# Optimization experiments

Hardware: AMD Instinct MI355X
Metric: run time of the kernel (lower is better)

## Reference

```python
import jax, jax.numpy as jnp
import numpy as np

B = 64          # batch size
KP1 = 1024      # K + 1 (negatives + positive)
D_IN = 2048     # inputSize
D_PROJ = 512    # proj_dim
N_MEM = 81920   # outputSize * f_Num
T = 0.07        # temperature
MOMENTUM = 0.5


def _l2norm(x):
    # Normalize(2): x / ||x||_2 along last dim
    return x / jnp.sqrt(jnp.sum(x * x, axis=-1, keepdims=True))


def setup_inputs() -> dict:
    key = jax.random.key(0)
    k1, k2, k3, k4, k5 = jax.random.split(key, 5)
    stdv = 1.0 / np.sqrt(D_IN / 3)
    feat = jax.random.normal(k1, (B, D_IN), jnp.float32)
    y = jax.random.randint(k2, (B,), 0, N_MEM, dtype=jnp.int32)
    idx = jax.random.randint(k3, (B, KP1), 0, N_MEM, dtype=jnp.int32)
    memory = jax.random.uniform(k4, (N_MEM, D_IN), jnp.float32, -stdv, stdv)
    W = jax.random.normal(k5, (D_PROJ, D_IN), jnp.float32) / np.sqrt(D_IN)
    b = jnp.zeros((D_PROJ,), jnp.float32)
    return {"feat": feat, "y": y, "idx": idx, "memory": memory, "W": W, "b": b}


def reference(feat, y, idx, memory, W, b):
    # project + l2-normalize query features: [B, D_PROJ]
    feat_proj = _l2norm(feat @ W.T + b)
    # gather bank rows (detached in original): [B*KP1, D_IN]
    weight = memory[idx.reshape(-1)]
    weight_proj = _l2norm(weight @ W.T + b).reshape(B, KP1, D_PROJ)
    # bmm([B,KP1,D_PROJ], [B,D_PROJ,1]) / T -> [B, KP1, 1]
    out = (jnp.einsum('bkd,bd->bk', weight_proj, feat_proj) / T)[..., None]
    # momentum scatter-update of memory rows at y
    new_rows = MOMENTUM * memory[y] + (1.0 - MOMENTUM) * feat
    new_memory = memory.at[y].set(new_rows)
    return out, new_memory
```

## Files before the change

kernel.cpp:

```cpp
#include <hip/hip_runtime.h>


#define B_SZ     64
#define KP1      1024
#define D_IN     2048
#define D_PROJ   512
#define N_MEM    81920
#define INV_T    (1.0f / 0.07f)

typedef __bf16 bf16x8 __attribute__((ext_vector_type(8)));
typedef float  f32x4  __attribute__((ext_vector_type(4)));

__device__ __forceinline__ unsigned short f2bf(float f) {
    unsigned int u = __float_as_uint(f);
    unsigned int r = (u + 0x7FFFu + ((u >> 16) & 1u)) >> 16;
    return (unsigned short)r;
}

__global__ void cvt_w_kernel(const float* __restrict__ W, unsigned short* __restrict__ Wb) {
    int i = blockIdx.x * 256 + threadIdx.x;
    float4 v = ((const float4*)W)[i];
    ushort4 o;
    o.x = f2bf(v.x); o.y = f2bf(v.y); o.z = f2bf(v.z); o.w = f2bf(v.w);
    ((ushort4*)Wb)[i] = o;
}

__global__ void feat_proj_kernel(const float* __restrict__ feat,
                                 const float* __restrict__ W,
                                 const float* __restrict__ bias,
                                 float* __restrict__ fp_out) {
    const int b = blockIdx.x, tid = threadIdx.x;
    __shared__ float sF[D_IN];
    __shared__ float sP[D_PROJ];
    __shared__ float sRed[256];

    #pragma unroll
    for (int i = 0; i < D_IN / 256; ++i)
        sF[tid + i * 256] = feat[(long)b * D_IN + tid + i * 256];
    __syncthreads();

    float pv[2];
    #pragma unroll
    for (int pass = 0; pass < 2; ++pass) {
        const int n = tid + pass * 256;
        const float4* wr = (const float4*)(W + (long)n * D_IN);
        const float4* fr = (const float4*)sF;
        float s = 0.f;
        for (int j = 0; j < D_IN / 4; ++j) {
            float4 wv = wr[j], fv = fr[j];
            s += wv.x * fv.x + wv.y * fv.y + wv.z * fv.z + wv.w * fv.w;
        }
        pv[pass] = s + bias[n];
        sP[n] = pv[pass];
    }
    __syncthreads();
    sRed[tid] = pv[0] * pv[0] + pv[1] * pv[1];
    __syncthreads();
    for (int s = 128; s > 0; s >>= 1) {
        if (tid < s) sRed[tid] += sRed[tid + s];
        __syncthreads();
    }
    const float rn = rsqrtf(sRed[0]);
    fp_out[(long)b * D_PROJ + tid]       = pv[0] * rn;
    fp_out[(long)b * D_PROJ + tid + 256] = pv[1] * rn;
}

#define AS_STRIDE 72
__global__ __launch_bounds__(256, 2)
void main_gemm_kernel(const float* __restrict__ memory,
                      const int* __restrict__ idx,
                      const unsigned short* __restrict__ Wb,
                      const float* __restrict__ fp,
                      const float* __restrict__ bias,
                      float* __restrict__ out) {
    const int tid  = threadIdx.x;
    const int w    = tid >> 6;
    const int lane = tid & 63;
    const int quad = lane >> 4;
    const int c16  = lane & 15;
    const int blk  = blockIdx.x;
    const int b    = blk >> 4;

    __shared__ unsigned short As[64 * AS_STRIDE];
    __shared__ float sFP[D_PROJ];
    __shared__ float sBias[D_PROJ];
    __shared__ int   sIdx[64];
    __shared__ float sSS[4 * 64];
    __shared__ float sDot[4 * 64];

    for (int i = tid; i < D_PROJ; i += 256) {
        sFP[i]   = fp[(long)b * D_PROJ + i];
        sBias[i] = bias[i];
    }
    if (tid < 64) sIdx[tid] = idx[blk * 64 + tid];
    __syncthreads();

    f32x4 acc[4][8];
    const f32x4 zero = {0.f, 0.f, 0.f, 0.f};
    #pragma unroll
    for (int mt = 0; mt < 4; ++mt)
        #pragma unroll
        for (int nt = 0; nt < 8; ++nt) acc[mt][nt] = zero;

    const int  row  = tid >> 2;
    const int  q    = tid & 3;
    const long arow = (long)sIdx[row] * D_IN;

    for (int k0 = 0; k0 < D_IN; k0 += 64) {
        const float4* src = (const float4*)(memory + arow + k0 + q * 16);
        float4 v0 = src[0], v1 = src[1], v2 = src[2], v3 = src[3];

        __syncthreads();
        float f[16] = {v0.x, v0.y, v0.z, v0.w, v1.x, v1.y, v1.z, v1.w,
                       v2.x, v2.y, v2.z, v2.w, v3.x, v3.y, v3.z, v3.w};
        unsigned int pk[8];
        #pragma unroll
        for (int j = 0; j < 8; ++j)
            pk[j] = (unsigned int)f2bf(f[2 * j]) | ((unsigned int)f2bf(f[2 * j + 1]) << 16);
        uint4* dst = (uint4*)&As[row * AS_STRIDE + q * 16];
        dst[0] = make_uint4(pk[0], pk[1], pk[2], pk[3]);
        dst[1] = make_uint4(pk[4], pk[5], pk[6], pk[7]);
        __syncthreads();

        #pragma unroll
        for (int ks = 0; ks < 2; ++ks) {
            bf16x8 af[4];
            #pragma unroll
            for (int mt = 0; mt < 4; ++mt)
                af[mt] = *(const bf16x8*)&As[(mt * 16 + c16) * AS_STRIDE + ks * 32 + quad * 8];
            #pragma unroll
            for (int nt = 0; nt < 8; ++nt) {
                const int n = w * 128 + nt * 16 + c16;
                bf16x8 bfr = *(const bf16x8*)&Wb[(long)n * D_IN + k0 + ks * 32 + quad * 8];
                #pragma unroll
                for (int mt = 0; mt < 4; ++mt)
                    acc[mt][nt] = __builtin_amdgcn_mfma_f32_16x16x32_bf16(
                        af[mt], bfr, acc[mt][nt], 0, 0, 0);
            }
        }
    }

    float ssl[4][4], dtl[4][4];
    #pragma unroll
    for (int mt = 0; mt < 4; ++mt)
        #pragma unroll
        for (int r = 0; r < 4; ++r) { ssl[mt][r] = 0.f; dtl[mt][r] = 0.f; }

    #pragma unroll
    for (int nt = 0; nt < 8; ++nt) {
        const int n = w * 128 + nt * 16 + c16;
        const float bv = sBias[n], fv = sFP[n];
        #pragma unroll
        for (int mt = 0; mt < 4; ++mt)
            #pragma unroll
            for (int r = 0; r < 4; ++r) {
                const float P = acc[mt][nt][r] + bv;
                ssl[mt][r] += P * P;
                dtl[mt][r] += P * fv;
            }
    }
    #pragma unroll
    for (int off = 8; off >= 1; off >>= 1)
        #pragma unroll
        for (int mt = 0; mt < 4; ++mt)
            #pragma unroll
            for (int r = 0; r < 4; ++r) {
                ssl[mt][r] += __shfl_xor(ssl[mt][r], off);
                dtl[mt][r] += __shfl_xor(dtl[mt][r], off);
            }
    if (c16 == 0) {
        #pragma unroll
        for (int mt = 0; mt < 4; ++mt)
            #pragma unroll
            for (int r = 0; r < 4; ++r) {
                const int rr = mt * 16 + quad * 4 + r;
                sSS[w * 64 + rr]  = ssl[mt][r];
                sDot[w * 64 + rr] = dtl[mt][r];
            }
    }
    __syncthreads();
    if (tid < 64) {
        const float ss = sSS[tid] + sSS[64 + tid] + sSS[128 + tid] + sSS[192 + tid];
        const float dt = sDot[tid] + sDot[64 + tid] + sDot[128 + tid] + sDot[192 + tid];
        out[blk * 64 + tid] = dt * rsqrtf(ss) * INV_T;
    }
}

__global__ void copy_mem_kernel(const float4* __restrict__ src,
                                float4* __restrict__ dst, long n4) {
    long i = (long)blockIdx.x * blockDim.x + threadIdx.x;
    const long stride = (long)gridDim.x * blockDim.x;
    for (; i < n4; i += stride) dst[i] = src[i];
}

__global__ void scatter_kernel(const float* __restrict__ memory,
                               const float* __restrict__ feat,
                               const int* __restrict__ y,
                               float* __restrict__ out_mem) {
    const int i  = blockIdx.x;
    const int yi = y[i];
    for (int j = i + 1; j < B_SZ; ++j)
        if (y[j] == yi) return;
    const float4* m4 = (const float4*)(memory + (long)yi * D_IN);
    const float4* f4 = (const float4*)(feat + (long)i * D_IN);
    float4* o4 = (float4*)(out_mem + (long)yi * D_IN);
    for (int c = threadIdx.x; c < D_IN / 4; c += 256) {
        float4 a = m4[c], b = f4[c];
        float4 r;
        r.x = 0.5f * (a.x + b.x); r.y = 0.5f * (a.y + b.y);
        r.z = 0.5f * (a.z + b.z); r.w = 0.5f * (a.w + b.w);
        o4[c] = r;
    }
}

extern "C" void kernel_launch(void* const* d_in, const int* in_sizes, int n_in,
                              void* d_out, int out_size, void* d_ws, size_t ws_size,
                              hipStream_t stream) {
    const float* feat   = (const float*)d_in[0];
    const int*   y      = (const int*)d_in[1];
    const int*   idx    = (const int*)d_in[2];
    const float* memory = (const float*)d_in[3];
    const float* W      = (const float*)d_in[4];
    const float* bias   = (const float*)d_in[5];

    float* out     = (float*)d_out;
    float* out_mem = out + (long)B_SZ * KP1;

    unsigned short* Wb = (unsigned short*)out_mem;
    float*          fp = out_mem + (long)D_PROJ * D_IN;

    cvt_w_kernel<<<(D_PROJ * D_IN) / (4 * 256), 256, 0, stream>>>(W, Wb);
    feat_proj_kernel<<<B_SZ, 256, 0, stream>>>(feat, W, bias, fp);
    main_gemm_kernel<<<(B_SZ * KP1) / 64, 256, 0, stream>>>(memory, idx, Wb, fp, bias, out);

    const long n4 = (long)N_MEM * D_IN / 4;
    copy_mem_kernel<<<32768, 256, 0, stream>>>((const float4*)memory, (float4*)out_mem, n4);
    scatter_kernel<<<B_SZ, 256, 0, stream>>>(memory, feat, y, out_mem);
}
```

Measured before the change: 1.483 ms.

## Project entire memory bank once and fuse the bank copy into projection

Instead of gathering 65536 indexed rows and projecting each, the kernel projects and normalizes all 81920 memory rows, writing the results to scratch space inside the output buffer. A small gather-dot kernel then looks up the normalized rows by idx and dots them with the query. The memory-bank copy to the output is folded into the projection's row loads, with a tail kernel copying only the rows that served as scratch. This trades about 25% more GEMM work for dropping one full read of the memory bank and the random-gather reads.

After: 1.685 ms. 1.14x slower.

```diff
diff --git a/kernel.cpp b/kernel.cpp
--- a/kernel.cpp
+++ b/kernel.cpp
@@ -7,6 +7,11 @@
 #define D_PROJ   512
 #define N_MEM    81920
 #define INV_T    (1.0f / 0.07f)
+
+#define PROJN_ROWS   20480
+#define TAIL_ROW     81648
+#define TAIL_ROWS    272
+#define COPY_SKIP    (TAIL_ROW - PROJN_ROWS)
 
 typedef __bf16 bf16x8 __attribute__((ext_vector_type(8)));
 typedef float  f32x4  __attribute__((ext_vector_type(4)));
@@ -67,33 +72,24 @@
 
 #define AS_STRIDE 72
 __global__ __launch_bounds__(256, 2)
-void main_gemm_kernel(const float* __restrict__ memory,
-                      const int* __restrict__ idx,
-                      const unsigned short* __restrict__ Wb,
-                      const float* __restrict__ fp,
-                      const float* __restrict__ bias,
-                      float* __restrict__ out) {
+void proj_all_kernel(const float* __restrict__ memory,
+                     const unsigned short* __restrict__ Wb,
+                     const float* __restrict__ bias,
+                     float* __restrict__ projn,
+                     float* __restrict__ out_mem) {
     const int tid  = threadIdx.x;
     const int w    = tid >> 6;
     const int lane = tid & 63;
     const int quad = lane >> 4;
     const int c16  = lane & 15;
-    const int blk  = blockIdx.x;
-    const int b    = blk >> 4;
+    const int r0   = blockIdx.x * 64;
 
     __shared__ unsigned short As[64 * AS_STRIDE];
-    __shared__ float sFP[D_PROJ];
     __shared__ float sBias[D_PROJ];
-    __shared__ int   sIdx[64];
     __shared__ float sSS[4 * 64];
-    __shared__ float sDot[4 * 64];
-
-    for (int i = tid; i < D_PROJ; i += 256) {
-        sFP[i]   = fp[(long)b * D_PROJ + i];
-        sBias[i] = bias[i];
-    }
-    if (tid < 64) sIdx[tid] = idx[blk * 64 + tid];
-    __syncthreads();
+    __shared__ float sInv[64];
+
+    for (int i = tid; i < D_PROJ; i += 256) sBias[i] = bias[i];
 
     f32x4 acc[4][8];
     const f32x4 zero = {0.f, 0.f, 0.f, 0.f};
@@ -104,11 +100,17 @@
 
     const int  row  = tid >> 2;
     const int  q    = tid & 3;
-    const long arow = (long)sIdx[row] * D_IN;
+    const int  grow = r0 + row;
+    const long arow = (long)grow * D_IN;
+    const bool do_copy = (grow >= PROJN_ROWS) & (grow < TAIL_ROW);
 
     for (int k0 = 0; k0 < D_IN; k0 += 64) {
         const float4* src = (const float4*)(memory + arow + k0 + q * 16);
         float4 v0 = src[0], v1 = src[1], v2 = src[2], v3 = src[3];
+        if (do_copy) {
+            float4* cdst = (float4*)(out_mem + arow + k0 + q * 16);
+            cdst[0] = v0; cdst[1] = v1; cdst[2] = v2; cdst[3] = v3;
+        }
 
         __syncthreads();
         float f[16] = {v0.x, v0.y, v0.z, v0.w, v1.x, v1.y, v1.z, v1.w,
@@ -140,23 +142,22 @@
         }
     }
 
-    float ssl[4][4], dtl[4][4];
+    float ssl[4][4];
     #pragma unroll
     for (int mt = 0; mt < 4; ++mt)
         #pragma unroll
-        for (int r = 0; r < 4; ++r) { ssl[mt][r] = 0.f; dtl[mt][r] = 0.f; }
+        for (int r = 0; r < 4; ++r) ssl[mt][r] = 0.f;
 
     #pragma unroll
     for (int nt = 0; nt < 8; ++nt) {
         const int n = w * 128 + nt * 16 + c16;
-        const float bv = sBias[n], fv = sFP[n];
+        const float bv = sBias[n];
         #pragma unroll
         for (int mt = 0; mt < 4; ++mt)
             #pragma unroll
             for (int r = 0; r < 4; ++r) {
                 const float P = acc[mt][nt][r] + bv;
                 ssl[mt][r] += P * P;
-                dtl[mt][r] += P * fv;
             }
     }
     #pragma unroll
@@ -164,33 +165,64 @@
         #pragma unroll
         for (int mt = 0; mt < 4; ++mt)
             #pragma unroll
-            for (int r = 0; r < 4; ++r) {
+            for (int r = 0; r < 4; ++r)
                 ssl[mt][r] += __shfl_xor(ssl[mt][r], off);
-                dtl[mt][r] += __shfl_xor(dtl[mt][r], off);
+    if (c16 == 0) {
+        #pragma unroll
+        for (int mt = 0; mt < 4; ++mt)
+            #pragma unroll
+            for (int r = 0; r < 4; ++r)
+                sSS[w * 64 + mt * 16 + quad * 4 + r] = ssl[mt][r];
+    }
+    __syncthreads();
+    if (tid < 64)
+        sInv[tid] = rsqrtf(sSS[tid] + sSS[64 + tid] + sSS[128 + tid] + sSS[192 + tid]);
+    __syncthreads();
+
+    #pragma unroll
+    for (int mt = 0; mt < 4; ++mt)
+        #pragma unroll
+        for (int r = 0; r < 4; ++r) {
+            const int  rr = mt * 16 + quad * 4 + r;
+            const float iv = sInv[rr];
+            const long base = (long)(r0 + rr) * D_PROJ;
+            #pragma unroll
+            for (int nt = 0; nt < 8; ++nt) {
+                const int n = w * 128 + nt * 16 + c16;
+                projn[base + n] = (acc[mt][nt][r] + sBias[n]) * iv;
             }
-    if (c16 == 0) {
-        #pragma unroll
-        for (int mt = 0; mt < 4; ++mt)
-            #pragma unroll
-            for (int r = 0; r < 4; ++r) {
-                const int rr = mt * 16 + quad * 4 + r;
-                sSS[w * 64 + rr]  = ssl[mt][r];
-                sDot[w * 64 + rr] = dtl[mt][r];
-            }
-    }
-    __syncthreads();
-    if (tid < 64) {
-        const float ss = sSS[tid] + sSS[64 + tid] + sSS[128 + tid] + sSS[192 + tid];
-        const float dt = sDot[tid] + sDot[64 + tid] + sDot[128 + tid] + sDot[192 + tid];
-        out[blk * 64 + tid] = dt * rsqrtf(ss) * INV_T;
-    }
-}
-
-__global__ void copy_mem_kernel(const float4* __restrict__ src,
-                                float4* __restrict__ dst, long n4) {
-    long i = (long)blockIdx.x * blockDim.x + threadIdx.x;
-    const long stride = (long)gridDim.x * blockDim.x;
-    for (; i < n4; i += stride) dst[i] = src[i];
+        }
+}
+
+__global__ void gather_dot_kernel(const int* __restrict__ idx,
+                                  const float* __restrict__ projn,
+                                  const float* __restrict__ fp,
+                                  float* __restrict__ out) {
+    const int tid  = threadIdx.x;
+    const int w    = tid >> 6;
+    const int lane = tid & 63;
+    const int e    = blockIdx.x * 4 + w;
+    const int b    = e >> 10;
+    const int row  = idx[e];
+    const float4* pr = (const float4*)(projn + (long)row * D_PROJ + lane * 8);
+    const float4* fr = (const float4*)(fp    + (long)b   * D_PROJ + lane * 8);
+    float4 p0 = pr[0], p1 = pr[1];
+    float4 f0 = fr[0], f1 = fr[1];
+    float s = p0.x * f0.x + p0.y * f0.y + p0.z * f0.z + p0.w * f0.w
+            + p1.x * f1.x + p1.y * f1.y + p1.z * f1.z + p1.w * f1.w;
+    #pragma unroll
+    for (int off = 32; off >= 1; off >>= 1) s += __shfl_xor(s, off);
+    if (lane == 0) out[e] = s * INV_T;
+}
+
+__global__ void tail_copy_kernel(const float4* __restrict__ src,
+                                 float4* __restrict__ dst) {
+    int r = blockIdx.x;
+    int row = (r < PROJN_ROWS) ? r : r + COPY_SKIP;
+    const long base = (long)row * (D_IN / 4);
+    const int c = threadIdx.x;
+    dst[base + c]       = src[base + c];
+    dst[base + c + 256] = src[base + c + 256];
 }
 
 __global__ void scatter_kernel(const float* __restrict__ memory,
@@ -226,14 +258,15 @@
     float* out     = (float*)d_out;
     float* out_mem = out + (long)B_SZ * KP1;
 
-    unsigned short* Wb = (unsigned short*)out_mem;
-    float*          fp = out_mem + (long)D_PROJ * D_IN;
+    float*          projn = out_mem;
+    unsigned short* Wb    = (unsigned short*)(out_mem + (long)TAIL_ROW * D_IN);
+    float*          fp    = out_mem + (long)TAIL_ROW * D_IN + (long)D_PROJ * D_IN / 2;
 
     cvt_w_kernel<<<(D_PROJ * D_IN) / (4 * 256), 256, 0, stream>>>(W, Wb);
     feat_proj_kernel<<<B_SZ, 256, 0, stream>>>(feat, W, bias, fp);
-    main_gemm_kernel<<<(B_SZ * KP1) / 64, 256, 0, stream>>>(memory, idx, Wb, fp, bias, out);
-
-    const long n4 = (long)N_MEM * D_IN / 4;
-    copy_mem_kernel<<<32768, 256, 0, stream>>>((const float4*)memory, (float4*)out_mem, n4);
+    proj_all_kernel<<<N_MEM / 64, 256, 0, stream>>>(memory, Wb, bias, projn, out_mem);
+    gather_dot_kernel<<<(B_SZ * KP1) / 4, 256, 0, stream>>>(idx, projn, fp, out);
+    tail_copy_kernel<<<PROJN_ROWS + TAIL_ROWS, 256, 0, stream>>>(
+        (const float4*)memory, (float4*)out_mem);
     scatter_kernel<<<B_SZ, 256, 0, stream>>>(memory, feat, y, out_mem);
 }
```
